# Kernel optimization log

Hardware: AMD Instinct MI355X
Metric: run time of the kernel (lower is better)

The kernel has to match this reference:

```python
import jax, jax.numpy as jnp
import numpy as np

N_NODES = 50000
N_EDGES = 400000
NODE_FEAT = 32
HIDDEN = 256
ACTION_DIM = 6
NUM_GRAPHS = 64


def setup_inputs() -> dict:
    key = jax.random.key(0)
    ks = jax.random.split(key, 9)
    x = jax.random.normal(ks[0], (N_NODES, NODE_FEAT), dtype=jnp.float32)
    edge_index = jax.random.randint(ks[1], (2, N_EDGES), 0, N_NODES, dtype=jnp.int32)
    batch = jnp.sort(jax.random.randint(ks[2], (N_NODES,), 0, NUM_GRAPHS, dtype=jnp.int32))
    # GCNConv weights (PyG stores Linear without bias + separate bias term;
    # here W is [in, out] so h = x @ W)
    s1 = 1.0 / np.sqrt(NODE_FEAT)
    s2 = 1.0 / np.sqrt(HIDDEN)
    W1 = jax.random.uniform(ks[3], (NODE_FEAT, HIDDEN), jnp.float32, -s1, s1)
    b1 = jnp.zeros((HIDDEN,), jnp.float32)
    W2 = jax.random.uniform(ks[4], (HIDDEN, HIDDEN), jnp.float32, -s2, s2)
    b2 = jnp.zeros((HIDDEN,), jnp.float32)
    Wf = jax.random.uniform(ks[5], (HIDDEN, 2 * ACTION_DIM), jnp.float32, -s2, s2)
    bf = jax.random.uniform(ks[6], (2 * ACTION_DIM,), jnp.float32, -s2, s2)
    return {"x": x, "edge_index": edge_index, "batch": batch,
            "W1": W1, "b1": b1, "W2": W2, "b2": b2, "Wf": Wf, "bf": bf}


def gcn_conv(x, src, dst, deg_inv_sqrt, W, b, num_nodes):
    # PyG GCNConv: h = x @ W, messages h[src] * norm scattered to dst, + bias.
    h = x @ W  # [N, out]
    norm = deg_inv_sqrt[src] * deg_inv_sqrt[dst]  # [E+N]
    msgs = h[src] * norm[:, None]  # [E+N, out]  (dominant memory traffic)
    out = jax.ops.segment_sum(msgs, dst, num_segments=num_nodes)
    return out + b


def reference(x, edge_index, batch, W1, b1, W2, b2, Wf, bf):
    num_nodes = x.shape[0]
    loop = jnp.arange(num_nodes, dtype=edge_index.dtype)
    src = jnp.concatenate([edge_index[0], loop])  # self-loops, PyG default
    dst = jnp.concatenate([edge_index[1], loop])
    deg = jax.ops.segment_sum(jnp.ones_like(dst, dtype=x.dtype), dst,
                              num_segments=num_nodes)  # >=1 due to self-loops
    deg_inv_sqrt = jax.lax.rsqrt(deg)

    h = jax.nn.relu(gcn_conv(x, src, dst, deg_inv_sqrt, W1, b1, num_nodes))
    h = jax.nn.relu(gcn_conv(h, src, dst, deg_inv_sqrt, W2, b2, num_nodes))

    # global_mean_pool over graph ids
    sums = jax.ops.segment_sum(h, batch, num_segments=NUM_GRAPHS)
    counts = jax.ops.segment_sum(jnp.ones((num_nodes,), x.dtype), batch,
                                 num_segments=NUM_GRAPHS)
    pooled = sums / jnp.maximum(counts, 1.0)[:, None]  # [G, HIDDEN]

    mls = pooled @ Wf + bf  # [G, 2*ACTION_DIM]
    mean, log_std = jnp.split(mls, 2, axis=-1)
    std = jnp.exp(jnp.clip(log_std, -20.0, 2.0))
    return mean, std
```

## Files before the change

### kernel.cpp

```cpp
#include <hip/hip_runtime.h>
#include <math.h>

#define NN 50000
#define FEAT 32
#define HID 256
#define NGRAPH 64
#define CAP 64

typedef __attribute__((ext_vector_type(8))) short bfrag;
typedef __attribute__((ext_vector_type(4))) float f32x4;

__device__ __forceinline__ float bf2f(unsigned short u) {
    union { unsigned int i; float f; } v; v.i = ((unsigned int)u) << 16; return v.f;
}
__device__ __forceinline__ unsigned short f2bf(float f) {
    union { float f; unsigned int i; } v; v.f = f;
    unsigned int r = v.i + 0x7fffu + ((v.i >> 16) & 1u);
    return (unsigned short)(r >> 16);
}

__device__ __forceinline__ void pack_w(const float* __restrict__ W,
                                       unsigned short* __restrict__ Wp, int K, int o) {
    int j    = o & 7;
    int lane = (o >> 3) & 63;
    int rest = o >> 9;
    int nst  = K >> 5;
    int ks   = rest & (nst - 1);
    int nb   = rest / nst;
    int n = nb * 16 + (lane & 15);
    int k = ks * 32 + (lane >> 4) * 8 + j;
    Wp[o] = f2bf(W[(size_t)k * HID + n]);
}

__global__ void k_prep(float4* __restrict__ zp, int n16,
                       const float* __restrict__ W1, const float* __restrict__ W2,
                       unsigned short* __restrict__ W1p, unsigned short* __restrict__ W2p) {
    int i = blockIdx.x * blockDim.x + threadIdx.x;
    if (i < n16) zp[i] = make_float4(0.f, 0.f, 0.f, 0.f);
    if (i < FEAT * HID) pack_w(W1, W1p, FEAT, i);
    int o2 = i - FEAT * HID;
    if (o2 >= 0 && o2 < HID * HID) pack_w(W2, W2p, HID, o2);
}

__global__ void k_setup(const int* __restrict__ src, const int* __restrict__ dst,
                        const int* __restrict__ batch,
                        int* __restrict__ counter, int* __restrict__ csr,
                        int* __restrict__ starts, int E, int N) {
    int e = blockIdx.x * blockDim.x + threadIdx.x;
    if (e < E) {
        int d = dst[e];
        int p = atomicAdd(&counter[d], 1);
        if (p < CAP) csr[d * CAP + p] = src[e];
    }
    if (e < N) {
        int b = batch[e];
        int prev = (e == 0) ? -1 : batch[e - 1];
        if (b != prev) {
            for (int g = prev + 1; g <= b; ++g) starts[g] = e;
        }
        if (e == N - 1) {
            for (int g = b + 1; g <= NGRAPH; ++g) starts[g] = N;
        }
    }
}

__global__ void k_disps(const float* __restrict__ x, const int* __restrict__ cnt,
                        float* __restrict__ dis, unsigned short* __restrict__ xp, int N) {
    int id = blockIdx.x * blockDim.x + threadIdx.x;
    if (id >= N * FEAT) return;
    int node = id >> 5;
    float dn = rsqrtf((float)(cnt[node] + 1));
    if ((id & 31) == 0) dis[node] = dn;
    xp[id] = f2bf(x[id] * dn);
}

__global__ void k_aggx(const unsigned short* __restrict__ xp, const int* __restrict__ cnt,
                       const int* __restrict__ csr, const float* __restrict__ dis,
                       unsigned short* __restrict__ out, int N) {
    int node = blockIdx.x * 8 + (threadIdx.x >> 5);
    if (node >= N) return;
    int col = threadIdx.x & 31;
    float acc = bf2f(xp[(size_t)node * FEAT + col]);
    int e = cnt[node]; if (e > CAP) e = CAP;
    const int* lst = &csr[(size_t)node * CAP];
    int i = 0;
    for (; i + 8 <= e; i += 8) {
        int4 sa = *(const int4*)&lst[i];
        int4 sb = *(const int4*)&lst[i + 4];
        float v0 = bf2f(xp[(size_t)sa.x * FEAT + col]);
        float v1 = bf2f(xp[(size_t)sa.y * FEAT + col]);
        float v2 = bf2f(xp[(size_t)sa.z * FEAT + col]);
        float v3 = bf2f(xp[(size_t)sa.w * FEAT + col]);
        float v4 = bf2f(xp[(size_t)sb.x * FEAT + col]);
        float v5 = bf2f(xp[(size_t)sb.y * FEAT + col]);
        float v6 = bf2f(xp[(size_t)sb.z * FEAT + col]);
        float v7 = bf2f(xp[(size_t)sb.w * FEAT + col]);
        acc += ((v0 + v1) + (v2 + v3)) + ((v4 + v5) + (v6 + v7));
    }
    for (; i + 4 <= e; i += 4) {
        int4 s4 = *(const int4*)&lst[i];
        float v0 = bf2f(xp[(size_t)s4.x * FEAT + col]);
        float v1 = bf2f(xp[(size_t)s4.y * FEAT + col]);
        float v2 = bf2f(xp[(size_t)s4.z * FEAT + col]);
        float v3 = bf2f(xp[(size_t)s4.w * FEAT + col]);
        acc += (v0 + v1) + (v2 + v3);
    }
    for (; i < e; ++i) acc += bf2f(xp[(size_t)lst[i] * FEAT + col]);
    out[(size_t)node * FEAT + col] = f2bf(acc * dis[node]);
}

__global__ void k_aggh(const unsigned short* __restrict__ h, const int* __restrict__ cnt,
                       const int* __restrict__ csr, const float* __restrict__ dis,
                       unsigned short* __restrict__ out, int N) {
    int gw = (int)((blockIdx.x * (size_t)blockDim.x + threadIdx.x) >> 6);
    int lane = threadIdx.x & 63;
    int node = gw * 2 + (lane >> 5);
    if (node >= N) return;
    int c0 = (lane & 31) * 8;

    bfrag sv = *(const bfrag*)&h[(size_t)node * HID + c0];
    float a[8];
#pragma unroll
    for (int j = 0; j < 8; ++j) a[j] = bf2f((unsigned short)sv[j]);

    int e = cnt[node]; if (e > CAP) e = CAP;
    const int* lst = &csr[(size_t)node * CAP];
    int i = 0;
    for (; i + 8 <= e; i += 8) {
        int4 sa = *(const int4*)&lst[i];
        int4 sb = *(const int4*)&lst[i + 4];
        bfrag w0 = *(const bfrag*)&h[(size_t)sa.x * HID + c0];
        bfrag w1 = *(const bfrag*)&h[(size_t)sa.y * HID + c0];
        bfrag w2 = *(const bfrag*)&h[(size_t)sa.z * HID + c0];
        bfrag w3 = *(const bfrag*)&h[(size_t)sa.w * HID + c0];
        bfrag w4 = *(const bfrag*)&h[(size_t)sb.x * HID + c0];
        bfrag w5 = *(const bfrag*)&h[(size_t)sb.y * HID + c0];
        bfrag w6 = *(const bfrag*)&h[(size_t)sb.z * HID + c0];
        bfrag w7 = *(const bfrag*)&h[(size_t)sb.w * HID + c0];
#pragma unroll
        for (int j = 0; j < 8; ++j) {
            a[j] += ((bf2f((unsigned short)w0[j]) + bf2f((unsigned short)w1[j]))
                   + (bf2f((unsigned short)w2[j]) + bf2f((unsigned short)w3[j])))
                  + ((bf2f((unsigned short)w4[j]) + bf2f((unsigned short)w5[j]))
                   + (bf2f((unsigned short)w6[j]) + bf2f((unsigned short)w7[j])));
        }
    }
    for (; i + 4 <= e; i += 4) {
        int4 s4 = *(const int4*)&lst[i];
        bfrag w0 = *(const bfrag*)&h[(size_t)s4.x * HID + c0];
        bfrag w1 = *(const bfrag*)&h[(size_t)s4.y * HID + c0];
        bfrag w2 = *(const bfrag*)&h[(size_t)s4.z * HID + c0];
        bfrag w3 = *(const bfrag*)&h[(size_t)s4.w * HID + c0];
#pragma unroll
        for (int j = 0; j < 8; ++j)
            a[j] += (bf2f((unsigned short)w0[j]) + bf2f((unsigned short)w1[j]))
                  + (bf2f((unsigned short)w2[j]) + bf2f((unsigned short)w3[j]));
    }
    for (; i < e; ++i) {
        bfrag w = *(const bfrag*)&h[(size_t)lst[i] * HID + c0];
#pragma unroll
        for (int j = 0; j < 8; ++j) a[j] += bf2f((unsigned short)w[j]);
    }
    float dn = dis[node];
    bfrag o;
#pragma unroll
    for (int j = 0; j < 8; ++j) o[j] = (short)f2bf(a[j] * dn);
    *(bfrag*)&out[(size_t)node * HID + c0] = o;
}

__global__ __launch_bounds__(256, 4)
void k_mmf(const unsigned short* __restrict__ A, const unsigned short* __restrict__ Wp,
           const float* __restrict__ bias, const float* __restrict__ scale,
           unsigned short* __restrict__ C, int M, int K, int lgK) {
    __shared__ unsigned short lds[64 * 264];
    int tid  = threadIdx.x;
    int lane = tid & 63;
    int wid  = tid >> 6;
    int l15  = lane & 15;
    int lq   = lane >> 4;
    int row0 = blockIdx.x * 64;

    const int P = K + 8;
    int iters = (64 * K) >> 11;
    for (int it = 0; it < iters; ++it) {
        int flat = (it * 256 + tid) * 8;
        int row = flat >> lgK;
        int col = flat & (K - 1);
        bfrag v = {0, 0, 0, 0, 0, 0, 0, 0};
        int gr = row0 + row;
        if (gr < M) v = *(const bfrag*)&A[(size_t)gr * K + col];
        *(bfrag*)&lds[row * P + col] = v;
    }
    __syncthreads();

    int nsteps = K >> 5;
    f32x4 acc[4][4];
#pragma unroll
    for (int mi = 0; mi < 4; ++mi)
#pragma unroll
        for (int ni = 0; ni < 4; ++ni) acc[mi][ni] = (f32x4){0.f, 0.f, 0.f, 0.f};

    for (int ks = 0; ks < nsteps; ++ks) {
        bfrag fb[4];
#pragma unroll
        for (int ni = 0; ni < 4; ++ni) {
            size_t off = (((size_t)(wid * 4 + ni) * nsteps + ks) * 64 + lane) * 8;
            fb[ni] = *(const bfrag*)&Wp[off];
        }
        bfrag fa[4];
        int koff = ks * 32 + lq * 8;
#pragma unroll
        for (int mi = 0; mi < 4; ++mi)
            fa[mi] = *(const bfrag*)&lds[(mi * 16 + l15) * P + koff];
#pragma unroll
        for (int mi = 0; mi < 4; ++mi)
#pragma unroll
            for (int ni = 0; ni < 4; ++ni)
                acc[mi][ni] = __builtin_amdgcn_mfma_f32_16x16x32_bf16(fb[ni], fa[mi], acc[mi][ni], 0, 0, 0);
    }

    float4 bv[4];
#pragma unroll
    for (int ni = 0; ni < 4; ++ni)
        bv[ni] = *(const float4*)&bias[(wid * 4 + ni) * 16 + lq * 4];
    float sv[4];
#pragma unroll
    for (int mi = 0; mi < 4; ++mi) {
        int gr = row0 + mi * 16 + l15;
        sv[mi] = (gr < M) ? scale[gr] : 0.f;
    }

    __syncthreads();
#pragma unroll
    for (int mi = 0; mi < 4; ++mi) {
#pragma unroll
        for (int ni = 0; ni < 4; ++ni) {
            const float* bp = (const float*)&bv[ni];
            ushort4 o;
            o.x = f2bf(fmaxf(acc[mi][ni][0] + bp[0], 0.f) * sv[mi]);
            o.y = f2bf(fmaxf(acc[mi][ni][1] + bp[1], 0.f) * sv[mi]);
            o.z = f2bf(fmaxf(acc[mi][ni][2] + bp[2], 0.f) * sv[mi]);
            o.w = f2bf(fmaxf(acc[mi][ni][3] + bp[3], 0.f) * sv[mi]);
            *(ushort4*)&lds[(mi * 16 + l15) * 264 + (wid * 4 + ni) * 16 + lq * 4] = o;
        }
    }
    __syncthreads();

#pragma unroll
    for (int i = 0; i < 8; ++i) {
        int F = (i * 256 + tid) * 8;
        int row = F >> 8;
        int col = F & 255;
        int gr = row0 + row;
        if (gr < M) {
            bfrag v = *(const bfrag*)&lds[row * 264 + col];
            *(bfrag*)&C[(size_t)gr * HID + col] = v;
        }
    }
}

__global__ __launch_bounds__(256, 4)
void k_mmfp(const unsigned short* __restrict__ A, const unsigned short* __restrict__ Wp,
            const float* __restrict__ bias, const int* __restrict__ batch,
            float* __restrict__ pooled, int M) {
    __shared__ unsigned short lds[64 * 264];
    __shared__ int bshare[64];
    const int K = HID;
    int tid  = threadIdx.x;
    int lane = tid & 63;
    int wid  = tid >> 6;
    int l15  = lane & 15;
    int lq   = lane >> 4;
    int row0 = blockIdx.x * 64;

    if (tid < 64) {
        int gr = row0 + tid;
        bshare[tid] = (gr < M) ? batch[gr] : -1;
    }

    const int P = K + 8;
    for (int it = 0; it < 8; ++it) {
        int flat = (it * 256 + tid) * 8;
        int row = flat >> 8;
        int col = flat & 255;
        bfrag v = {0, 0, 0, 0, 0, 0, 0, 0};
        int gr = row0 + row;
        if (gr < M) v = *(const bfrag*)&A[(size_t)gr * K + col];
        *(bfrag*)&lds[row * P + col] = v;
    }
    __syncthreads();

    f32x4 acc[4][4];
#pragma unroll
    for (int mi = 0; mi < 4; ++mi)
#pragma unroll
        for (int ni = 0; ni < 4; ++ni) acc[mi][ni] = (f32x4){0.f, 0.f, 0.f, 0.f};

    for (int ks = 0; ks < 8; ++ks) {
        bfrag fb[4];
#pragma unroll
        for (int ni = 0; ni < 4; ++ni) {
            size_t off = (((size_t)(wid * 4 + ni) * 8 + ks) * 64 + lane) * 8;
            fb[ni] = *(const bfrag*)&Wp[off];
        }
        bfrag fa[4];
        int koff = ks * 32 + lq * 8;
#pragma unroll
        for (int mi = 0; mi < 4; ++mi)
            fa[mi] = *(const bfrag*)&lds[(mi * 16 + l15) * P + koff];
#pragma unroll
        for (int mi = 0; mi < 4; ++mi)
#pragma unroll
            for (int ni = 0; ni < 4; ++ni)
                acc[mi][ni] = __builtin_amdgcn_mfma_f32_16x16x32_bf16(fb[ni], fa[mi], acc[mi][ni], 0, 0, 0);
    }

    float4 bv[4];
#pragma unroll
    for (int ni = 0; ni < 4; ++ni)
        bv[ni] = *(const float4*)&bias[(wid * 4 + ni) * 16 + lq * 4];

    __syncthreads();
#pragma unroll
    for (int mi = 0; mi < 4; ++mi) {
#pragma unroll
        for (int ni = 0; ni < 4; ++ni) {
            const float* bp = (const float*)&bv[ni];
            ushort4 o;
            o.x = f2bf(fmaxf(acc[mi][ni][0] + bp[0], 0.f));
            o.y = f2bf(fmaxf(acc[mi][ni][1] + bp[1], 0.f));
            o.z = f2bf(fmaxf(acc[mi][ni][2] + bp[2], 0.f));
            o.w = f2bf(fmaxf(acc[mi][ni][3] + bp[3], 0.f));
            *(ushort4*)&lds[(mi * 16 + l15) * 264 + (wid * 4 + ni) * 16 + lq * 4] = o;
        }
    }
    __syncthreads();

    int c = tid;
    float pacc = 0.f;
    int cur = bshare[0];
    for (int r = 0; r < 64; ++r) {
        int g = bshare[r];
        if (g != cur) {
            if (cur >= 0) atomicAdd(&pooled[(size_t)cur * HID + c], pacc);
            pacc = 0.f; cur = g;
        }
        pacc += bf2f(lds[r * 264 + c]);
    }
    if (cur >= 0) atomicAdd(&pooled[(size_t)cur * HID + c], pacc);
}

__global__ void k_head(const float* __restrict__ pooled, const int* __restrict__ starts,
                       const float* __restrict__ Wf, const float* __restrict__ bf,
                       float* __restrict__ out) {
    int t = blockIdx.x * blockDim.x + threadIdx.x;
    if (t >= NGRAPH * 12) return;
    int g = t / 12, j = t % 12;
    float cntf = (float)(starts[g + 1] - starts[g]);
    float inv = 1.f / fmaxf(cntf, 1.f);
    float s = 0.f;
    for (int k = 0; k < HID; ++k) s += pooled[(size_t)g * HID + k] * Wf[k * 12 + j];
    s = s * inv + bf[j];
    if (j < 6) {
        out[g * 6 + j] = s;
    } else {
        float ls = fminf(fmaxf(s, -20.f), 2.f);
        out[NGRAPH * 6 + g * 6 + (j - 6)] = expf(ls);
    }
}

extern "C" void kernel_launch(void* const* d_in, const int* in_sizes, int n_in,
                              void* d_out, int out_size, void* d_ws, size_t ws_size,
                              hipStream_t stream) {
    const float* x     = (const float*)d_in[0];
    const int*   ei    = (const int*)d_in[1];
    const int*   batch = (const int*)d_in[2];
    const float* W1    = (const float*)d_in[3];
    const float* b1    = (const float*)d_in[4];
    const float* W2    = (const float*)d_in[5];
    const float* b2    = (const float*)d_in[6];
    const float* Wf    = (const float*)d_in[7];
    const float* bfv   = (const float*)d_in[8];
    float* out = (float*)d_out;

    const int E = in_sizes[1] / 2;
    const int N = in_sizes[2];
    const int* srcp = ei;
    const int* dstp = ei + E;

    char* ws = (char*)d_ws;
    const size_t OFF_CTR    = 0;
    const size_t OFF_POOLED = 200192;
    const size_t OFF_STARTS = 265728;
    const size_t OFF_DIS    = 266240;
    const size_t OFF_W1P    = 466432;
    const size_t OFF_W2P    = 482816;
    const size_t OFF_CSR    = 613888;
    const size_t OFF_XP     = 13413888;
    const size_t OFF_AGGX   = 16613888;
    const size_t OFF_H1     = 19813888;
    const size_t OFF_G      = 45413888;

    int*            ctr    = (int*)(ws + OFF_CTR);
    float*          pooled = (float*)(ws + OFF_POOLED);
    int*            starts = (int*)(ws + OFF_STARTS);
    float*          dis    = (float*)(ws + OFF_DIS);
    unsigned short* W1p    = (unsigned short*)(ws + OFF_W1P);
    unsigned short* W2p    = (unsigned short*)(ws + OFF_W2P);
    int*            csr    = (int*)(ws + OFF_CSR);
    unsigned short* xp     = (unsigned short*)(ws + OFF_XP);
    unsigned short* aggX   = (unsigned short*)(ws + OFF_AGGX);
    unsigned short* h1     = (unsigned short*)(ws + OFF_H1);
    unsigned short* g      = (unsigned short*)(ws + OFF_G);

    const int T = 256;
    const int prep_n = (FEAT + HID) * HID;
    k_prep<<<(prep_n + T - 1) / T, T, 0, stream>>>((float4*)ws, 265728 / 16, W1, W2, W1p, W2p);
    k_setup<<<(E + T - 1) / T, T, 0, stream>>>(srcp, dstp, batch, ctr, csr, starts, E, N);
    k_disps<<<(N * FEAT + T - 1) / T, T, 0, stream>>>(x, ctr, dis, xp, N);

    k_aggx<<<(N + 7) / 8, T, 0, stream>>>(xp, ctr, csr, dis, aggX, N);
    k_mmf<<<(N + 63) / 64, T, 0, stream>>>(aggX, W1p, b1, dis, h1, N, FEAT, 5);

    k_aggh<<<(N + 7) / 8, T, 0, stream>>>(h1, ctr, csr, dis, g, N);
    k_mmfp<<<(N + 63) / 64, T, 0, stream>>>(g, W2p, b2, batch, pooled, N);

    k_head<<<3, T, 0, stream>>>(pooled, starts, Wf, bfv, out);
}
```

Baseline: 126.6 us.

## Fuse degree scaling into aggregation, store CSR as 16-bit indices, shrink cap

Removes the separate k_disps kernel and the dis/xp buffers. The layer-1 aggregation now reads fp32 x directly and recomputes rsqrt of neighbour degrees on the fly, and the GEMM epilogue recomputes the scale from the counts. Neighbour lists are stored as 16-bit indices (node count below 65536) with the per-node cap lowered from 64 to 48, which halves index traffic. The costs are extra gathers of cnt[] for every neighbour in the first layer, and dropped edges if any node has more than 48 in-edges. The GEMM is also specialised to K=32.

```diff
diff --git a/kernel.cpp b/kernel.cpp
--- a/kernel.cpp
+++ b/kernel.cpp
@@ -5,9 +5,10 @@
 #define FEAT 32
 #define HID 256
 #define NGRAPH 64
-#define CAP 64
+#define CAP 48
 
 typedef __attribute__((ext_vector_type(8))) short bfrag;
+typedef __attribute__((ext_vector_type(8))) unsigned short u16x8;
 typedef __attribute__((ext_vector_type(4))) float f32x4;
 
 __device__ __forceinline__ float bf2f(unsigned short u) {
@@ -44,13 +45,13 @@
 
 __global__ void k_setup(const int* __restrict__ src, const int* __restrict__ dst,
                         const int* __restrict__ batch,
-                        int* __restrict__ counter, int* __restrict__ csr,
+                        int* __restrict__ counter, unsigned short* __restrict__ csr,
                         int* __restrict__ starts, int E, int N) {
     int e = blockIdx.x * blockDim.x + threadIdx.x;
     if (e < E) {
         int d = dst[e];
         int p = atomicAdd(&counter[d], 1);
-        if (p < CAP) csr[d * CAP + p] = src[e];
+        if (p < CAP) csr[(size_t)d * CAP + p] = (unsigned short)src[e];
     }
     if (e < N) {
         int b = batch[e];
@@ -64,53 +65,47 @@
     }
 }
 
-__global__ void k_disps(const float* __restrict__ x, const int* __restrict__ cnt,
-                        float* __restrict__ dis, unsigned short* __restrict__ xp, int N) {
-    int id = blockIdx.x * blockDim.x + threadIdx.x;
-    if (id >= N * FEAT) return;
-    int node = id >> 5;
-    float dn = rsqrtf((float)(cnt[node] + 1));
-    if ((id & 31) == 0) dis[node] = dn;
-    xp[id] = f2bf(x[id] * dn);
-}
-
-__global__ void k_aggx(const unsigned short* __restrict__ xp, const int* __restrict__ cnt,
-                       const int* __restrict__ csr, const float* __restrict__ dis,
+__global__ void k_aggx(const float* __restrict__ x, const int* __restrict__ cnt,
+                       const unsigned short* __restrict__ csr,
                        unsigned short* __restrict__ out, int N) {
     int node = blockIdx.x * 8 + (threadIdx.x >> 5);
     if (node >= N) return;
     int col = threadIdx.x & 31;
-    float acc = bf2f(xp[(size_t)node * FEAT + col]);
-    int e = cnt[node]; if (e > CAP) e = CAP;
-    const int* lst = &csr[(size_t)node * CAP];
+    int ecnt = cnt[node];
+    float dn = rsqrtf((float)(ecnt + 1));
+    int e = ecnt > CAP ? CAP : ecnt;
+    const unsigned short* lst = &csr[(size_t)node * CAP];
+
+    float acc = x[(size_t)node * FEAT + col] * dn;
     int i = 0;
     for (; i + 8 <= e; i += 8) {
-        int4 sa = *(const int4*)&lst[i];
-        int4 sb = *(const int4*)&lst[i + 4];
-        float v0 = bf2f(xp[(size_t)sa.x * FEAT + col]);
-        float v1 = bf2f(xp[(size_t)sa.y * FEAT + col]);
-        float v2 = bf2f(xp[(size_t)sa.z * FEAT + col]);
-        float v3 = bf2f(xp[(size_t)sa.w * FEAT + col]);
-        float v4 = bf2f(xp[(size_t)sb.x * FEAT + col]);
-        float v5 = bf2f(xp[(size_t)sb.y * FEAT + col]);
-        float v6 = bf2f(xp[(size_t)sb.z * FEAT + col]);
-        float v7 = bf2f(xp[(size_t)sb.w * FEAT + col]);
-        acc += ((v0 + v1) + (v2 + v3)) + ((v4 + v5) + (v6 + v7));
+        u16x8 s = *(const u16x8*)&lst[i];
+        float vs[8];
+#pragma unroll
+        for (int j = 0; j < 8; ++j) {
+            int sj = (int)s[j];
+            vs[j] = x[(size_t)sj * FEAT + col] * rsqrtf((float)(cnt[sj] + 1));
+        }
+        acc += ((vs[0] + vs[1]) + (vs[2] + vs[3])) + ((vs[4] + vs[5]) + (vs[6] + vs[7]));
     }
     for (; i + 4 <= e; i += 4) {
-        int4 s4 = *(const int4*)&lst[i];
-        float v0 = bf2f(xp[(size_t)s4.x * FEAT + col]);
-        float v1 = bf2f(xp[(size_t)s4.y * FEAT + col]);
-        float v2 = bf2f(xp[(size_t)s4.z * FEAT + col]);
-        float v3 = bf2f(xp[(size_t)s4.w * FEAT + col]);
-        acc += (v0 + v1) + (v2 + v3);
-    }
-    for (; i < e; ++i) acc += bf2f(xp[(size_t)lst[i] * FEAT + col]);
-    out[(size_t)node * FEAT + col] = f2bf(acc * dis[node]);
+        float vs[4];
+#pragma unroll
+        for (int j = 0; j < 4; ++j) {
+            int sj = (int)lst[i + j];
+            vs[j] = x[(size_t)sj * FEAT + col] * rsqrtf((float)(cnt[sj] + 1));
+        }
+        acc += (vs[0] + vs[1]) + (vs[2] + vs[3]);
+    }
+    for (; i < e; ++i) {
+        int sj = (int)lst[i];
+        acc += x[(size_t)sj * FEAT + col] * rsqrtf((float)(cnt[sj] + 1));
+    }
+    out[(size_t)node * FEAT + col] = f2bf(acc * dn);
 }
 
 __global__ void k_aggh(const unsigned short* __restrict__ h, const int* __restrict__ cnt,
-                       const int* __restrict__ csr, const float* __restrict__ dis,
+                       const unsigned short* __restrict__ csr,
                        unsigned short* __restrict__ out, int N) {
     int gw = (int)((blockIdx.x * (size_t)blockDim.x + threadIdx.x) >> 6);
     int lane = threadIdx.x & 63;
@@ -118,25 +113,27 @@
     if (node >= N) return;
     int c0 = (lane & 31) * 8;
 
+    int ecnt = cnt[node];
+    float dn = rsqrtf((float)(ecnt + 1));
+    int e = ecnt > CAP ? CAP : ecnt;
+    const unsigned short* lst = &csr[(size_t)node * CAP];
+
     bfrag sv = *(const bfrag*)&h[(size_t)node * HID + c0];
     float a[8];
 #pragma unroll
     for (int j = 0; j < 8; ++j) a[j] = bf2f((unsigned short)sv[j]);
 
-    int e = cnt[node]; if (e > CAP) e = CAP;
-    const int* lst = &csr[(size_t)node * CAP];
     int i = 0;
     for (; i + 8 <= e; i += 8) {
-        int4 sa = *(const int4*)&lst[i];
-        int4 sb = *(const int4*)&lst[i + 4];
-        bfrag w0 = *(const bfrag*)&h[(size_t)sa.x * HID + c0];
-        bfrag w1 = *(const bfrag*)&h[(size_t)sa.y * HID + c0];
-        bfrag w2 = *(const bfrag*)&h[(size_t)sa.z * HID + c0];
-        bfrag w3 = *(const bfrag*)&h[(size_t)sa.w * HID + c0];
-        bfrag w4 = *(const bfrag*)&h[(size_t)sb.x * HID + c0];
-        bfrag w5 = *(const bfrag*)&h[(size_t)sb.y * HID + c0];
-        bfrag w6 = *(const bfrag*)&h[(size_t)sb.z * HID + c0];
-        bfrag w7 = *(const bfrag*)&h[(size_t)sb.w * HID + c0];
+        u16x8 s = *(const u16x8*)&lst[i];
+        bfrag w0 = *(const bfrag*)&h[(size_t)s[0] * HID + c0];
+        bfrag w1 = *(const bfrag*)&h[(size_t)s[1] * HID + c0];
+        bfrag w2 = *(const bfrag*)&h[(size_t)s[2] * HID + c0];
+        bfrag w3 = *(const bfrag*)&h[(size_t)s[3] * HID + c0];
+        bfrag w4 = *(const bfrag*)&h[(size_t)s[4] * HID + c0];
+        bfrag w5 = *(const bfrag*)&h[(size_t)s[5] * HID + c0];
+        bfrag w6 = *(const bfrag*)&h[(size_t)s[6] * HID + c0];
+        bfrag w7 = *(const bfrag*)&h[(size_t)s[7] * HID + c0];
 #pragma unroll
         for (int j = 0; j < 8; ++j) {
             a[j] += ((bf2f((unsigned short)w0[j]) + bf2f((unsigned short)w1[j]))
@@ -146,11 +143,10 @@
         }
     }
     for (; i + 4 <= e; i += 4) {
-        int4 s4 = *(const int4*)&lst[i];
-        bfrag w0 = *(const bfrag*)&h[(size_t)s4.x * HID + c0];
-        bfrag w1 = *(const bfrag*)&h[(size_t)s4.y * HID + c0];
-        bfrag w2 = *(const bfrag*)&h[(size_t)s4.z * HID + c0];
-        bfrag w3 = *(const bfrag*)&h[(size_t)s4.w * HID + c0];
+        bfrag w0 = *(const bfrag*)&h[(size_t)lst[i]     * HID + c0];
+        bfrag w1 = *(const bfrag*)&h[(size_t)lst[i + 1] * HID + c0];
+        bfrag w2 = *(const bfrag*)&h[(size_t)lst[i + 2] * HID + c0];
+        bfrag w3 = *(const bfrag*)&h[(size_t)lst[i + 3] * HID + c0];
 #pragma unroll
         for (int j = 0; j < 8; ++j)
             a[j] += (bf2f((unsigned short)w0[j]) + bf2f((unsigned short)w1[j]))
@@ -161,7 +157,6 @@
 #pragma unroll
         for (int j = 0; j < 8; ++j) a[j] += bf2f((unsigned short)w[j]);
     }
-    float dn = dis[node];
     bfrag o;
 #pragma unroll
     for (int j = 0; j < 8; ++j) o[j] = (short)f2bf(a[j] * dn);
@@ -170,9 +165,10 @@
 
 __global__ __launch_bounds__(256, 4)
 void k_mmf(const unsigned short* __restrict__ A, const unsigned short* __restrict__ Wp,
-           const float* __restrict__ bias, const float* __restrict__ scale,
-           unsigned short* __restrict__ C, int M, int K, int lgK) {
+           const float* __restrict__ bias, const int* __restrict__ cnt,
+           unsigned short* __restrict__ C, int M) {
     __shared__ unsigned short lds[64 * 264];
+    const int K = FEAT;
     int tid  = threadIdx.x;
     int lane = tid & 63;
     int wid  = tid >> 6;
@@ -181,11 +177,10 @@
     int row0 = blockIdx.x * 64;
 
     const int P = K + 8;
-    int iters = (64 * K) >> 11;
-    for (int it = 0; it < iters; ++it) {
-        int flat = (it * 256 + tid) * 8;
-        int row = flat >> lgK;
-        int col = flat & (K - 1);
+    {
+        int flat = tid * 8;
+        int row = flat >> 5;
+        int col = flat & 31;
         bfrag v = {0, 0, 0, 0, 0, 0, 0, 0};
         int gr = row0 + row;
         if (gr < M) v = *(const bfrag*)&A[(size_t)gr * K + col];
@@ -193,31 +188,27 @@
     }
     __syncthreads();
 
-    int nsteps = K >> 5;
     f32x4 acc[4][4];
 #pragma unroll
     for (int mi = 0; mi < 4; ++mi)
 #pragma unroll
         for (int ni = 0; ni < 4; ++ni) acc[mi][ni] = (f32x4){0.f, 0.f, 0.f, 0.f};
 
-    for (int ks = 0; ks < nsteps; ++ks) {
-        bfrag fb[4];
-#pragma unroll
-        for (int ni = 0; ni < 4; ++ni) {
-            size_t off = (((size_t)(wid * 4 + ni) * nsteps + ks) * 64 + lane) * 8;
-            fb[ni] = *(const bfrag*)&Wp[off];
-        }
-        bfrag fa[4];
-        int koff = ks * 32 + lq * 8;
-#pragma unroll
-        for (int mi = 0; mi < 4; ++mi)
-            fa[mi] = *(const bfrag*)&lds[(mi * 16 + l15) * P + koff];
-#pragma unroll
-        for (int mi = 0; mi < 4; ++mi)
-#pragma unroll
-            for (int ni = 0; ni < 4; ++ni)
-                acc[mi][ni] = __builtin_amdgcn_mfma_f32_16x16x32_bf16(fb[ni], fa[mi], acc[mi][ni], 0, 0, 0);
-    }
+    bfrag fb[4];
+#pragma unroll
+    for (int ni = 0; ni < 4; ++ni) {
+        size_t off = (((size_t)(wid * 4 + ni)) * 64 + lane) * 8;
+        fb[ni] = *(const bfrag*)&Wp[off];
+    }
+    bfrag fa[4];
+#pragma unroll
+    for (int mi = 0; mi < 4; ++mi)
+        fa[mi] = *(const bfrag*)&lds[(mi * 16 + l15) * P + lq * 8];
+#pragma unroll
+    for (int mi = 0; mi < 4; ++mi)
+#pragma unroll
+        for (int ni = 0; ni < 4; ++ni)
+            acc[mi][ni] = __builtin_amdgcn_mfma_f32_16x16x32_bf16(fb[ni], fa[mi], acc[mi][ni], 0, 0, 0);
 
     float4 bv[4];
 #pragma unroll
@@ -227,7 +218,7 @@
 #pragma unroll
     for (int mi = 0; mi < 4; ++mi) {
         int gr = row0 + mi * 16 + l15;
-        sv[mi] = (gr < M) ? scale[gr] : 0.f;
+        sv[mi] = (gr < M) ? rsqrtf((float)(cnt[gr] + 1)) : 0.f;
     }
 
     __syncthreads();
@@ -391,24 +382,21 @@
     char* ws = (char*)d_ws;
     const size_t OFF_CTR    = 0;
     const size_t OFF_POOLED = 200192;
+    const size_t ZERO_BYTES = 265728;
     const size_t OFF_STARTS = 265728;
-    const size_t OFF_DIS    = 266240;
-    const size_t OFF_W1P    = 466432;
-    const size_t OFF_W2P    = 482816;
-    const size_t OFF_CSR    = 613888;
-    const size_t OFF_XP     = 13413888;
-    const size_t OFF_AGGX   = 16613888;
-    const size_t OFF_H1     = 19813888;
-    const size_t OFF_G      = 45413888;
+    const size_t OFF_W1P    = 266240;
+    const size_t OFF_W2P    = 282624;
+    const size_t OFF_CSR    = 413696;
+    const size_t OFF_AGGX   = 5213696;
+    const size_t OFF_H1     = 8413696;
+    const size_t OFF_G      = 34013696;
 
     int*            ctr    = (int*)(ws + OFF_CTR);
     float*          pooled = (float*)(ws + OFF_POOLED);
     int*            starts = (int*)(ws + OFF_STARTS);
-    float*          dis    = (float*)(ws + OFF_DIS);
     unsigned short* W1p    = (unsigned short*)(ws + OFF_W1P);
     unsigned short* W2p    = (unsigned short*)(ws + OFF_W2P);
-    int*            csr    = (int*)(ws + OFF_CSR);
-    unsigned short* xp     = (unsigned short*)(ws + OFF_XP);
+    unsigned short* csr    = (unsigned short*)(ws + OFF_CSR);
     unsigned short* aggX   = (unsigned short*)(ws + OFF_AGGX);
     unsigned short* h1     = (unsigned short*)(ws + OFF_H1);
     unsigned short* g      = (unsigned short*)(ws + OFF_G);
@@ -417,12 +405,11 @@
     const int prep_n = (FEAT + HID) * HID;
     k_prep<<<(prep_n + T - 1) / T, T, 0, stream>>>((float4*)ws, 265728 / 16, W1, W2, W1p, W2p);
     k_setup<<<(E + T - 1) / T, T, 0, stream>>>(srcp, dstp, batch, ctr, csr, starts, E, N);
-    k_disps<<<(N * FEAT + T - 1) / T, T, 0, stream>>>(x, ctr, dis, xp, N);
-
-    k_aggx<<<(N + 7) / 8, T, 0, stream>>>(xp, ctr, csr, dis, aggX, N);
-    k_mmf<<<(N + 63) / 64, T, 0, stream>>>(aggX, W1p, b1, dis, h1, N, FEAT, 5);
-
-    k_aggh<<<(N + 7) / 8, T, 0, stream>>>(h1, ctr, csr, dis, g, N);
+
+    k_aggx<<<(N + 7) / 8, T, 0, stream>>>(x, ctr, csr, aggX, N);
+    k_mmf<<<(N + 63) / 64, T, 0, stream>>>(aggX, W1p, b1, ctr, h1, N);
+
+    k_aggh<<<(N + 7) / 8, T, 0, stream>>>(h1, ctr, csr, g, N);
     k_mmfp<<<(N + 63) / 64, T, 0, stream>>>(g, W2p, b2, batch, pooled, N);
 
     k_head<<<3, T, 0, stream>>>(pooled, starts, Wf, bfv, out);
```

New measurement: 121.2 us. -4.3%, faster.
